# Kernel tuning notes

Measured on AMD Instinct MI355X. Metric: run time of the kernel, lower is better.

## Reference

```python
import jax, jax.numpy as jnp
import numpy as np

B, N_PER, E_PER = 128, 512, 8192          # graphs, nodes/graph, edges/graph
NUM_FEAT, NUM_REL, NUM_BASES = 4, 5, 2
LATENT = [32, 32, 32, 32]
D = 128                                    # sum(LATENT)
MAXN = 50                                  # self.max_neighbor
MAX_WALKS = 21
NUM_CLASSES = 5


def setup_inputs() -> dict:
    key = jax.random.key(0)
    ks = jax.random.split(key, 16)
    N, E = B * N_PER, B * E_PER
    # one-hot node-label features; node 0 of each graph = target user ([1,0,0,0]),
    # node 1 = target item ([0,1,0,0]), rest labels in {2,3}
    labels = jax.random.randint(ks[0], (B, N_PER), 2, NUM_FEAT)
    labels = labels.at[:, 0].set(0).at[:, 1].set(1)
    x = jax.nn.one_hot(labels.reshape(-1), NUM_FEAT, dtype=jnp.float32)
    offs = (jnp.arange(B, dtype=jnp.int32) * N_PER)[:, None]
    src = (jax.random.randint(ks[1], (B, E_PER), 0, N_PER).astype(jnp.int32) + offs).reshape(-1)
    dst = (jax.random.randint(ks[2], (B, E_PER), 0, N_PER).astype(jnp.int32) + offs).reshape(-1)
    edge_index = jnp.stack([src, dst])                       # [2, E] graph-local blocks
    edge_type = jax.random.randint(ks[3], (E,), 0, NUM_REL).astype(jnp.int32)
    batch = jnp.repeat(jnp.arange(B, dtype=jnp.int32), N_PER)
    inp = dict(x=x, edge_index=edge_index, edge_type=edge_type, batch=batch)
    dims = [NUM_FEAT] + LATENT
    ki = 4
    for l in range(4):
        fin, fout = dims[l], dims[l + 1]
        s = 1.0 / np.sqrt(fin)
        inp[f"basis{l}"] = (jax.random.normal(ks[ki], (NUM_BASES, fin, fout)) * s).astype(jnp.float32)
        inp[f"comp{l}"] = (jax.random.normal(ks[ki + 1], (NUM_REL, NUM_BASES)) * 0.5).astype(jnp.float32)
        inp[f"root{l}"] = (jax.random.normal(ks[ki + 2], (fin, fout)) * s).astype(jnp.float32)
        inp[f"cbias{l}"] = jnp.zeros((fout,), jnp.float32)
        ki += 3
    k2 = jax.random.split(jax.random.key(1), 4)
    inp["walk_w"] = (jax.random.normal(k2[0], (MAXN, D)) / np.sqrt(D)).astype(jnp.float32)
    inp["walk_b"] = jnp.zeros((MAXN,), jnp.float32)
    inp["lin1_w"] = (jax.random.normal(k2[1], (128, D)) / np.sqrt(D)).astype(jnp.float32)
    inp["lin1_b"] = jnp.zeros((128,), jnp.float32)
    inp["lin2_w"] = (jax.random.normal(k2[2], (NUM_CLASSES, 128)) / np.sqrt(128.0)).astype(jnp.float32)
    inp["lin2_b"] = jnp.zeros((NUM_CLASSES,), jnp.float32)
    return inp


def _rgcn(h, src, dst, etype, basis, comp, root, bias, n):
    # RGCNConv with basis decomposition: W_r = sum_b comp[r,b] * basis[b]; mean aggregation.
    hs = h[src]                                   # [E, fin]
    ce = comp[etype]                              # [E, num_bases]
    msg = ce[:, 0:1] * (hs @ basis[0])
    for b in range(1, NUM_BASES):
        msg = msg + ce[:, b:b + 1] * (hs @ basis[b])
    agg = jax.ops.segment_sum(msg, dst, num_segments=n)
    deg = jax.ops.segment_sum(jnp.ones(src.shape, msg.dtype), dst, num_segments=n)
    return agg / jnp.maximum(deg, 1.0)[:, None] + h @ root + bias


def _neighbor_table(src, dst, n):
    # per-node sorted out-neighbor lists, padded to MAXN with sentinel n
    E = src.shape[0]
    order = jnp.lexsort((dst, src))               # sort by src, then dst (== torch.sort of neighbors)
    s, d = src[order], dst[order]
    deg = jax.ops.segment_sum(jnp.ones((E,), jnp.int32), src, num_segments=n)
    offs = jnp.cumsum(deg) - deg
    rank = jnp.arange(E, dtype=jnp.int32) - offs[s]
    col = jnp.where(rank < MAXN, rank, MAXN)      # overflow -> dummy column
    table = jnp.full((n, MAXN + 1), n, jnp.int32).at[s, col].set(d)
    return table[:, :MAXN], deg


def _walk(xg, nbr, deg, start, end, w, b):
    # naive_reasoning_walking for one graph: xg [n,D], nbr [n,MAXN] local (pad=n), deg [n]
    n = xg.shape[0]
    trav0 = jnp.zeros((n,), bool).at[start].set(True)

    def step(state, _):
        node, acc, trav, done = state
        nb = jnp.clip(nbr[node], 0, n - 1)        # pads clipped; masked out below
        cnt = deg[node]
        no_nbr = cnt == 0
        logits = w @ acc + b                      # naive_walking_lin1(accumulated)
        valid = (jnp.arange(MAXN) < cnt) & ~trav[nb]
        sel = nb[jnp.argmax(jnp.where(valid, logits, -jnp.inf))]
        acc_new = acc + jnp.where(no_nbr, xg[end], xg[sel])
        upd = ~done
        move = upd & ~no_nbr
        acc = jnp.where(upd, acc_new, acc)
        trav = jnp.where(move, trav.at[sel].set(True), trav)
        done = done | (upd & (no_nbr | (sel == end)))
        node = jnp.where(move, sel, node)
        return (node, acc, trav, done), None

    (_, acc, trav, _), _ = jax.lax.scan(
        step, (start, xg[start], trav0, jnp.array(False)), None, length=MAX_WALKS)
    return acc / trav.sum().astype(acc.dtype)


def _forward(x, edge_index, edge_type, convs, walk_w, walk_b, lin1_w, lin1_b, lin2_w, lin2_b):
    N = x.shape[0]
    src, dst = edge_index[0], edge_index[1]
    h, states = x, []
    for basis, comp, root, bias in convs:
        h = jnp.tanh(_rgcn(h, src, dst, edge_type, basis, comp, root, bias, N))
        states.append(h)
    cs = jnp.concatenate(states, axis=1)          # [N, 128]
    table, deg = _neighbor_table(src, dst, N)
    # graphs are equal-sized (N_PER nodes each) -> per-graph local view
    tab = table.reshape(B, N_PER, MAXN)
    goff = (jnp.arange(B, dtype=jnp.int32) * N_PER)[:, None, None]
    tab_l = jnp.where(tab == N, N_PER, tab - goff)
    deg_l = deg.reshape(B, N_PER)
    xg = cs.reshape(B, N_PER, -1)
    start_l = jnp.argmax(x[:, 0].reshape(B, N_PER), axis=1)   # target user per graph
    end_l = jnp.argmax(x[:, 1].reshape(B, N_PER), axis=1)     # target item per graph
    pooled = jax.vmap(_walk, in_axes=(0, 0, 0, 0, 0, None, None))(
        xg, tab_l, deg_l, start_l, end_l, walk_w, walk_b)      # [B, 128]
    hid = jax.nn.relu(pooled @ lin1_w.T + lin1_b)              # dropout off (eval)
    logits = hid @ lin2_w.T + lin2_b
    return jax.nn.log_softmax(logits, axis=-1)


def reference(x, edge_index, edge_type, batch,
              basis0, comp0, root0, cbias0, basis1, comp1, root1, cbias1,
              basis2, comp2, root2, cbias2, basis3, comp3, root3, cbias3,
              walk_w, walk_b, lin1_w, lin1_b, lin2_w, lin2_b):
    # batch is implied by the fixed graph size; kept for interface fidelity
    convs = [(basis0, comp0, root0, cbias0), (basis1, comp1, root1, cbias1),
             (basis2, comp2, root2, cbias2), (basis3, comp3, root3, cbias3)]
    return _forward(x, edge_index, edge_type, convs,
                    walk_w, walk_b, lin1_w, lin1_b, lin2_w, lin2_b)
```

## Files before the change

kernel.cpp:

```cpp
#include <hip/hip_runtime.h>
#include <math.h>

#define NGRAPH 128
#define NPER   512
#define EPER   8192
#define NFEAT  4
#define NREL   5
#define DD     128
#define MAXNB  50
#define MAXW   21
#define NCLS   5

typedef unsigned short ushortT;
typedef unsigned char ucharT;

#define NTA 1024

__device__ __forceinline__ void scanExcl(const int* cnt, int* offs, int* tA,
                                         int* tB, int tid) {
  if (tid < NPER) tA[tid] = cnt[tid];
  __syncthreads();
  int* a = tA; int* b = tB;
  for (int d = 1; d < NPER; d <<= 1) {
    if (tid < NPER) {
      int v = a[tid];
      if (tid >= d) v += a[tid - d];
      b[tid] = v;
    }
    __syncthreads();
    int* t = a; a = b; b = t;
  }
  if (tid < NPER) offs[tid] = a[tid] - cnt[tid];
  __syncthreads();
}

__global__ __launch_bounds__(NTA, 1)
void build_csr2(const int* __restrict__ esrc, const int* __restrict__ edst,
                const int* __restrict__ etype, const float* __restrict__ x,
                ushortT* __restrict__ gBin, ushortT* __restrict__ gOut,
                int* __restrict__ pIn, int* __restrict__ pOut,
                int* __restrict__ gSE) {
  __shared__ int keyS[EPER];
  __shared__ int auxS[EPER];
  __shared__ ushortT nodS[EPER];
  __shared__ ucharT etyS[EPER];
  __shared__ int cnt[NPER], offs[NPER], fill[NPER];
  __shared__ int se[2];
  const int bid = blockIdx.x, tid = threadIdx.x;
  const int half = bid >> 7;
  const int g = bid & 127;
  const int nbase = g * NPER, ebase = g * EPER;

  if (tid < NPER) { cnt[tid] = 0; fill[tid] = 0; }
  if (tid < 2) se[tid] = NPER;
  __syncthreads();

  if (half == 0) {
    for (int e = tid; e < EPER; e += NTA) {
      auxS[e] = esrc[ebase + e] - nbase;
      etyS[e] = (ucharT)etype[ebase + e];
      int d = edst[ebase + e] - nbase;
      atomicAdd(&cnt[d], 1);
    }
    __syncthreads();
    scanExcl(cnt, offs, keyS, keyS + NPER, tid);
    for (int e = tid; e < EPER; e += NTA) {
      int d = edst[ebase + e] - nbase;
      int pos = offs[d] + atomicAdd(&fill[d], 1);
      keyS[pos] = (d << 13) | e;
    }
    __syncthreads();
    for (int p = tid; p < EPER; p += NTA) {
      const int k = keyS[p];
      const int n = k >> 13;
      const int o = offs[n], c = cnt[n];
      int r = 0;
      for (int i = 0; i < c; ++i) r += (keyS[o + i] < k);
      const int e = k & (EPER - 1);
      gBin[(size_t)g * EPER + o + r] = (ushortT)((auxS[e] << 3) | (int)etyS[e]);
    }
    if (tid < NPER) pIn[nbase + tid] = (offs[tid] << 14) | cnt[tid];
  } else {
    for (int e = tid; e < EPER; e += NTA) {
      int s = esrc[ebase + e] - nbase;
      auxS[e] = s;
      atomicAdd(&cnt[s], 1);
    }
    if (tid < NPER) {
      if (x[(size_t)(nbase + tid) * NFEAT + 0] > 0.5f) atomicMin(&se[0], tid);
      if (x[(size_t)(nbase + tid) * NFEAT + 1] > 0.5f) atomicMin(&se[1], tid);
    }
    __syncthreads();
    scanExcl(cnt, offs, keyS, keyS + NPER, tid);
    for (int e = tid; e < EPER; e += NTA) {
      int s = auxS[e];
      int d = edst[ebase + e] - nbase;
      int pos = offs[s] + atomicAdd(&fill[s], 1);
      keyS[pos] = (d << 13) | e;
      nodS[pos] = (ushortT)s;
    }
    __syncthreads();
    for (int p = tid; p < EPER; p += NTA) {
      const int k = keyS[p];
      const int n = (int)nodS[p];
      const int o = offs[n], c = cnt[n];
      int r = 0;
      for (int i = 0; i < c; ++i) r += (keyS[o + i] < k);
      gOut[(size_t)g * EPER + o + r] = (ushortT)(k >> 13);
    }
    if (tid < NPER) pOut[nbase + tid] = (offs[tid] << 14) | cnt[tid];
    if (tid < 2) gSE[g * 2 + tid] = (se[tid] >= NPER) ? 0 : se[tid];
  }
}

template <int FIN>
__global__ __launch_bounds__(512, 1)
void rgcn_layer2(const float* __restrict__ x, float* __restrict__ cs,
                 const ushortT* __restrict__ gBin, const int* __restrict__ pIn,
                 const float* __restrict__ bas, const float* __restrict__ cmp,
                 const float* __restrict__ rt, const float* __restrict__ bi,
                 int l) {
  constexpr int NK4 = (3 * FIN) / 4;
  constexpr int LPN = FIN / 4;
  __shared__ float A_s[NK4 * 256 * 4];
  __shared__ float Bt_s[NK4 * 32 * 4];
  __shared__ float compS[NREL * 2];
  const int bid = blockIdx.x, tid = threadIdx.x;
  const int g = bid >> 1, half = bid & 1;
  const int nbase = g * NPER;
  const int nb2 = nbase + half * 256;

  for (int idx = tid; idx < NK4 * 128; idx += 512) {
    const int k4 = idx >> 7, rem = idx & 127;
    const int o = rem >> 2, c = rem & 3;
    const int k = k4 * 4 + c;
    float v;
    if (k < FIN) v = bas[k * 32 + o];
    else if (k < 2 * FIN) v = bas[(FIN + (k - FIN)) * 32 + o];
    else v = rt[(k - 2 * FIN) * 32 + o];
    Bt_s[(k4 * 32 + o) * 4 + c] = v;
  }
  if (tid < NREL * 2) compS[tid] = cmp[tid];
  for (int idx = tid; idx < 256 * LPN; idx += 512) {
    const int n = idx / LPN, kq = idx % LPN;
    float4 hv;
    if constexpr (FIN == 4)
      hv = *(const float4*)(x + (size_t)(nb2 + n) * NFEAT);
    else
      hv = *(const float4*)(cs + (size_t)(nb2 + n) * DD + (l - 1) * 32 + kq * 4);
    *(float4*)&A_s[((2 * LPN + kq) * 256 + n) * 4] = hv;
  }
  __syncthreads();

  for (int t = tid; t < 256 * LPN; t += 512) {
    const int n = t / LPN, q = t % LPN;
    const int pk = pIn[nb2 + n];
    const int off = pk >> 14, c = pk & 16383;
    const float inv = 1.0f / (float)(c > 1 ? c : 1);
    float4 s0 = make_float4(0.f, 0.f, 0.f, 0.f);
    float4 s1 = make_float4(0.f, 0.f, 0.f, 0.f);
    const ushortT* el = gBin + (size_t)g * EPER + off;
    for (int i = 0; i < c; ++i) {
      const int pe = (int)el[i];
      const int s = pe >> 3, r = pe & 7;
      float4 hv;
      if constexpr (FIN == 4)
        hv = *(const float4*)(x + (size_t)(nbase + s) * NFEAT);
      else
        hv = *(const float4*)(cs + (size_t)(nbase + s) * DD + (l - 1) * 32 + q * 4);
      const float c0 = compS[r * 2 + 0], c1 = compS[r * 2 + 1];
      s0.x = fmaf(c0, hv.x, s0.x); s0.y = fmaf(c0, hv.y, s0.y);
      s0.z = fmaf(c0, hv.z, s0.z); s0.w = fmaf(c0, hv.w, s0.w);
      s1.x = fmaf(c1, hv.x, s1.x); s1.y = fmaf(c1, hv.y, s1.y);
      s1.z = fmaf(c1, hv.z, s1.z); s1.w = fmaf(c1, hv.w, s1.w);
    }
    s0.x *= inv; s0.y *= inv; s0.z *= inv; s0.w *= inv;
    s1.x *= inv; s1.y *= inv; s1.z *= inv; s1.w *= inv;
    *(float4*)&A_s[(q * 256 + n) * 4] = s0;
    *(float4*)&A_s[((LPN + q) * 256 + n) * 4] = s1;
  }
  __syncthreads();

  const int ot = (tid >> 4) & 3;
  const int nt = (tid & 15) | ((tid >> 6) << 4);
  const int n0 = 2 * nt, o0 = 8 * ot;
  float acc[2][8];
#pragma unroll
  for (int i = 0; i < 2; ++i)
#pragma unroll
    for (int j = 0; j < 8; ++j) acc[i][j] = 0.f;
  for (int k4 = 0; k4 < NK4; ++k4) {
    const float4 a0 = *(const float4*)&A_s[(k4 * 256 + n0) * 4];
    const float4 a1 = *(const float4*)&A_s[(k4 * 256 + n0 + 1) * 4];
#pragma unroll
    for (int j = 0; j < 8; ++j) {
      const float4 b = *(const float4*)&Bt_s[(k4 * 32 + o0 + j) * 4];
      acc[0][j] = fmaf(a0.x, b.x, acc[0][j]);
      acc[0][j] = fmaf(a0.y, b.y, acc[0][j]);
      acc[0][j] = fmaf(a0.z, b.z, acc[0][j]);
      acc[0][j] = fmaf(a0.w, b.w, acc[0][j]);
      acc[1][j] = fmaf(a1.x, b.x, acc[1][j]);
      acc[1][j] = fmaf(a1.y, b.y, acc[1][j]);
      acc[1][j] = fmaf(a1.z, b.z, acc[1][j]);
      acc[1][j] = fmaf(a1.w, b.w, acc[1][j]);
    }
  }
#pragma unroll
  for (int i = 0; i < 2; ++i) {
    float4 w0, w1;
    w0.x = tanhf(acc[i][0] + bi[o0 + 0]); w0.y = tanhf(acc[i][1] + bi[o0 + 1]);
    w0.z = tanhf(acc[i][2] + bi[o0 + 2]); w0.w = tanhf(acc[i][3] + bi[o0 + 3]);
    w1.x = tanhf(acc[i][4] + bi[o0 + 4]); w1.y = tanhf(acc[i][5] + bi[o0 + 5]);
    w1.z = tanhf(acc[i][6] + bi[o0 + 6]); w1.w = tanhf(acc[i][7] + bi[o0 + 7]);
    float* dst = cs + (size_t)(nb2 + n0 + i) * DD + l * 32 + o0;
    *(float4*)dst = w0;
    *(float4*)(dst + 4) = w1;
  }
}

__global__ __launch_bounds__(256, 1)
void walk_head(const float* __restrict__ cs, const ushortT* __restrict__ gOut,
               const int* __restrict__ pOut, const int* __restrict__ gSE,
               const float* __restrict__ walk_w, const float* __restrict__ walk_b,
               const float* __restrict__ lin1_w, const float* __restrict__ lin1_b,
               const float* __restrict__ lin2_w, const float* __restrict__ lin2_b,
               float* __restrict__ out) {
  __shared__ float wT[DD * 65];
  __shared__ float wb[64];
  __shared__ float accS[DD];
  __shared__ float part[4 * 64];
  __shared__ int trav[NPER];
  __shared__ float pooledS[DD], hidS[DD], logitsS[8];
  __shared__ int scal[8];
  const int g = blockIdx.x, tid = threadIdx.x;
  const int nbase = g * NPER;

  for (int i = tid; i < DD * 64; i += 256) {
    const int j = i >> 7, k = i & 127;
    wT[k * 65 + j] = walk_w[j * DD + k];
  }
  if (tid < 64) {
    wb[tid] = (tid < MAXNB) ? walk_b[tid] : 0.f;
    for (int k = 0; k < DD; ++k)
      if (tid >= MAXNB) wT[k * 65 + tid] = 0.f;
  }
  for (int i = tid; i < NPER; i += 256) trav[i] = 0;
  __syncthreads();
  const int startN = gSE[2 * g];
  const int endN = gSE[2 * g + 1];
  if (tid == 0) { scal[0] = startN; scal[1] = 0; scal[6] = 0; trav[startN] = 1; }
  if (tid < DD) accS[tid] = cs[(size_t)(nbase + startN) * DD + tid];
  __syncthreads();

  for (int step = 0; step < MAXW; ++step) {
    {
      const int w = tid >> 6, j = tid & 63, k0 = w * 32;
      float s = 0.f;
#pragma unroll
      for (int k = 0; k < 32; ++k) s += wT[(k0 + k) * 65 + j] * accS[k0 + k];
      part[w * 64 + j] = s;
    }
    __syncthreads();
    if (tid < 64) {
      const int j = tid;
      float lg = part[j] + part[64 + j] + part[128 + j] + part[192 + j];
      lg += wb[j];
      const int node = scal[0];
      const int pk = pOut[nbase + node];
      const int off = pk >> 14, c = pk & 16383;
      const int jmax = (c < MAXNB) ? c : MAXNB;
      float myval = -INFINITY;
      if (j < jmax) {
        const int nb = (int)gOut[(size_t)g * EPER + off + j];
        if (!trav[nb]) myval = lg;
      }
      int myidx = j;
#pragma unroll
      for (int o = 1; o < 64; o <<= 1) {
        const float ov = __shfl_xor(myval, o, 64);
        const int oi = __shfl_xor(myidx, o, 64);
        if (ov > myval || (ov == myval && oi < myidx)) { myval = ov; myidx = oi; }
      }
      if (j == 0) {
        const int done = scal[1];
        const int no_nbr = (c == 0);
        int sel = no_nbr ? (NPER - 1) : (int)gOut[(size_t)g * EPER + off + myidx];
        const int upd = !done;
        const int move = upd && !no_nbr;
        scal[2] = upd;
        scal[3] = no_nbr ? endN : sel;
        if (move) trav[sel] = 1;
        if (upd && (no_nbr || sel == endN)) scal[1] = 1;
        if (move) scal[0] = sel;
      }
    }
    __syncthreads();
    if (scal[2] && tid < DD) accS[tid] += cs[(size_t)(nbase + scal[3]) * DD + tid];
    __syncthreads();
  }

  for (int i = tid; i < NPER; i += 256)
    if (trav[i]) atomicAdd(&scal[6], 1);
  __syncthreads();
  {
    const float tc = (float)scal[6];
    if (tid < DD) pooledS[tid] = accS[tid] / tc;
  }
  __syncthreads();
  if (tid < DD) {
    const float4* w4 = (const float4*)(lin1_w + (size_t)tid * DD);
    float s = lin1_b[tid];
#pragma unroll 8
    for (int k4 = 0; k4 < DD / 4; ++k4) {
      const float4 wv = w4[k4];
      s += wv.x * pooledS[k4 * 4 + 0] + wv.y * pooledS[k4 * 4 + 1]
         + wv.z * pooledS[k4 * 4 + 2] + wv.w * pooledS[k4 * 4 + 3];
    }
    hidS[tid] = fmaxf(s, 0.f);
  }
  __syncthreads();
  if (tid < NCLS) {
    const float4* w4 = (const float4*)(lin2_w + (size_t)tid * DD);
    float s = lin2_b[tid];
#pragma unroll 8
    for (int k4 = 0; k4 < DD / 4; ++k4) {
      const float4 wv = w4[k4];
      s += wv.x * hidS[k4 * 4 + 0] + wv.y * hidS[k4 * 4 + 1]
         + wv.z * hidS[k4 * 4 + 2] + wv.w * hidS[k4 * 4 + 3];
    }
    logitsS[tid] = s;
  }
  __syncthreads();
  if (tid < NCLS) {
    float m = logitsS[0];
    for (int c = 1; c < NCLS; ++c) m = fmaxf(m, logitsS[c]);
    float sum = 0.f;
    for (int c = 0; c < NCLS; ++c) sum += expf(logitsS[c] - m);
    const float lse = m + logf(sum);
    out[g * NCLS + tid] = logitsS[tid] - lse;
  }
}

extern "C" void kernel_launch(void* const* d_in, const int* in_sizes, int n_in,
                              void* d_out, int out_size, void* d_ws, size_t ws_size,
                              hipStream_t stream) {
  const float* x = (const float*)d_in[0];
  const int* ei = (const int*)d_in[1];
  const int E = in_sizes[1] / 2;
  const int* esrc = ei;
  const int* edst = ei + E;
  const int* et = (const int*)d_in[2];

  char* ws = (char*)d_ws;
  float* cs = (float*)ws;
  size_t off = (size_t)NGRAPH * NPER * DD * sizeof(float);
  ushortT* gBin = (ushortT*)(ws + off); off += (size_t)NGRAPH * EPER * sizeof(ushortT);
  ushortT* gOut = (ushortT*)(ws + off); off += (size_t)NGRAPH * EPER * sizeof(ushortT);
  int* pIn = (int*)(ws + off); off += (size_t)NGRAPH * NPER * sizeof(int);
  int* pOut = (int*)(ws + off); off += (size_t)NGRAPH * NPER * sizeof(int);
  int* gSE = (int*)(ws + off); off += (size_t)NGRAPH * 2 * sizeof(int);

  build_csr2<<<dim3(2 * NGRAPH), dim3(NTA), 0, stream>>>(esrc, edst, et, x, gBin,
                                                         gOut, pIn, pOut, gSE);
  rgcn_layer2<NFEAT><<<dim3(2 * NGRAPH), dim3(512), 0, stream>>>(
      x, cs, gBin, pIn, (const float*)d_in[4], (const float*)d_in[5],
      (const float*)d_in[6], (const float*)d_in[7], 0);
  rgcn_layer2<32><<<dim3(2 * NGRAPH), dim3(512), 0, stream>>>(
      x, cs, gBin, pIn, (const float*)d_in[8], (const float*)d_in[9],
      (const float*)d_in[10], (const float*)d_in[11], 1);
  rgcn_layer2<32><<<dim3(2 * NGRAPH), dim3(512), 0, stream>>>(
      x, cs, gBin, pIn, (const float*)d_in[12], (const float*)d_in[13],
      (const float*)d_in[14], (const float*)d_in[15], 2);
  rgcn_layer2<32><<<dim3(2 * NGRAPH), dim3(512), 0, stream>>>(
      x, cs, gBin, pIn, (const float*)d_in[16], (const float*)d_in[17],
      (const float*)d_in[18], (const float*)d_in[19], 3);
  walk_head<<<dim3(NGRAPH), dim3(256), 0, stream>>>(
      cs, gOut, pOut, gSE, (const float*)d_in[20], (const float*)d_in[21],
      (const float*)d_in[22], (const float*)d_in[23], (const float*)d_in[24],
      (const float*)d_in[25], (float*)d_out);
}
```

Measured before the change: 178.6 us.

## Split RGCN layers into smaller blocks, unroll gathers, prefetch walk candidates

The RGCN layer kernel now processes 64 nodes per 256-thread block (8 blocks per graph) instead of 256 nodes per 512-thread block, giving more blocks and better occupancy. The neighbor gather loop is unrolled by four so several loads are in flight at once. The walk kernel stages its graph's CSR arrays in shared memory and prefetches all candidate neighbor feature rows into a scratch buffer while the logits matvec runs, which takes the dependent global read off the serial per-step critical path. It also skips that work once the walk is done. The cost is much more shared memory per walk block and redundant prefetch traffic for neighbors that are not chosen.

```diff
diff --git a/kernel.cpp b/kernel.cpp
--- a/kernel.cpp
+++ b/kernel.cpp
@@ -113,46 +113,46 @@
   }
 }
 
+#define NPB 64
 template <int FIN>
-__global__ __launch_bounds__(512, 1)
-void rgcn_layer2(const float* __restrict__ x, float* __restrict__ cs,
+__global__ __launch_bounds__(256)
+void rgcn_layer3(const float* __restrict__ x, float* __restrict__ cs,
                  const ushortT* __restrict__ gBin, const int* __restrict__ pIn,
                  const float* __restrict__ bas, const float* __restrict__ cmp,
                  const float* __restrict__ rt, const float* __restrict__ bi,
                  int l) {
   constexpr int NK4 = (3 * FIN) / 4;
   constexpr int LPN = FIN / 4;
-  __shared__ float A_s[NK4 * 256 * 4];
+  __shared__ float A_s[NK4 * NPB * 4];
   __shared__ float Bt_s[NK4 * 32 * 4];
   __shared__ float compS[NREL * 2];
   const int bid = blockIdx.x, tid = threadIdx.x;
-  const int g = bid >> 1, half = bid & 1;
+  const int g = bid >> 3, blk = bid & 7;
   const int nbase = g * NPER;
-  const int nb2 = nbase + half * 256;
-
-  for (int idx = tid; idx < NK4 * 128; idx += 512) {
+  const int nb2 = nbase + blk * NPB;
+
+  for (int idx = tid; idx < NK4 * 128; idx += 256) {
     const int k4 = idx >> 7, rem = idx & 127;
     const int o = rem >> 2, c = rem & 3;
     const int k = k4 * 4 + c;
     float v;
-    if (k < FIN) v = bas[k * 32 + o];
-    else if (k < 2 * FIN) v = bas[(FIN + (k - FIN)) * 32 + o];
+    if (k < 2 * FIN) v = bas[k * 32 + o];
     else v = rt[(k - 2 * FIN) * 32 + o];
     Bt_s[(k4 * 32 + o) * 4 + c] = v;
   }
   if (tid < NREL * 2) compS[tid] = cmp[tid];
-  for (int idx = tid; idx < 256 * LPN; idx += 512) {
+  for (int idx = tid; idx < NPB * LPN; idx += 256) {
     const int n = idx / LPN, kq = idx % LPN;
     float4 hv;
     if constexpr (FIN == 4)
       hv = *(const float4*)(x + (size_t)(nb2 + n) * NFEAT);
     else
       hv = *(const float4*)(cs + (size_t)(nb2 + n) * DD + (l - 1) * 32 + kq * 4);
-    *(float4*)&A_s[((2 * LPN + kq) * 256 + n) * 4] = hv;
-  }
-  __syncthreads();
-
-  for (int t = tid; t < 256 * LPN; t += 512) {
+    *(float4*)&A_s[((2 * LPN + kq) * NPB + n) * 4] = hv;
+  }
+  __syncthreads();
+
+  for (int t = tid; t < NPB * LPN; t += 256) {
     const int n = t / LPN, q = t % LPN;
     const int pk = pIn[nb2 + n];
     const int off = pk >> 14, c = pk & 16383;
@@ -160,15 +160,44 @@
     float4 s0 = make_float4(0.f, 0.f, 0.f, 0.f);
     float4 s1 = make_float4(0.f, 0.f, 0.f, 0.f);
     const ushortT* el = gBin + (size_t)g * EPER + off;
-    for (int i = 0; i < c; ++i) {
+    const float* hb;
+    int stride;
+    if constexpr (FIN == 4) { hb = x + (size_t)nbase * NFEAT; stride = NFEAT; }
+    else { hb = cs + (size_t)nbase * DD + (l - 1) * 32 + q * 4; stride = DD; }
+    int i = 0;
+    for (; i + 4 <= c; i += 4) {
+      const int p0 = (int)el[i + 0], p1 = (int)el[i + 1];
+      const int p2 = (int)el[i + 2], p3 = (int)el[i + 3];
+      const float4 h0 = *(const float4*)(hb + (size_t)(p0 >> 3) * stride);
+      const float4 h1 = *(const float4*)(hb + (size_t)(p1 >> 3) * stride);
+      const float4 h2 = *(const float4*)(hb + (size_t)(p2 >> 3) * stride);
+      const float4 h3 = *(const float4*)(hb + (size_t)(p3 >> 3) * stride);
+      float c0, c1;
+      c0 = compS[(p0 & 7) * 2]; c1 = compS[(p0 & 7) * 2 + 1];
+      s0.x = fmaf(c0, h0.x, s0.x); s0.y = fmaf(c0, h0.y, s0.y);
+      s0.z = fmaf(c0, h0.z, s0.z); s0.w = fmaf(c0, h0.w, s0.w);
+      s1.x = fmaf(c1, h0.x, s1.x); s1.y = fmaf(c1, h0.y, s1.y);
+      s1.z = fmaf(c1, h0.z, s1.z); s1.w = fmaf(c1, h0.w, s1.w);
+      c0 = compS[(p1 & 7) * 2]; c1 = compS[(p1 & 7) * 2 + 1];
+      s0.x = fmaf(c0, h1.x, s0.x); s0.y = fmaf(c0, h1.y, s0.y);
+      s0.z = fmaf(c0, h1.z, s0.z); s0.w = fmaf(c0, h1.w, s0.w);
+      s1.x = fmaf(c1, h1.x, s1.x); s1.y = fmaf(c1, h1.y, s1.y);
+      s1.z = fmaf(c1, h1.z, s1.z); s1.w = fmaf(c1, h1.w, s1.w);
+      c0 = compS[(p2 & 7) * 2]; c1 = compS[(p2 & 7) * 2 + 1];
+      s0.x = fmaf(c0, h2.x, s0.x); s0.y = fmaf(c0, h2.y, s0.y);
+      s0.z = fmaf(c0, h2.z, s0.z); s0.w = fmaf(c0, h2.w, s0.w);
+      s1.x = fmaf(c1, h2.x, s1.x); s1.y = fmaf(c1, h2.y, s1.y);
+      s1.z = fmaf(c1, h2.z, s1.z); s1.w = fmaf(c1, h2.w, s1.w);
+      c0 = compS[(p3 & 7) * 2]; c1 = compS[(p3 & 7) * 2 + 1];
+      s0.x = fmaf(c0, h3.x, s0.x); s0.y = fmaf(c0, h3.y, s0.y);
+      s0.z = fmaf(c0, h3.z, s0.z); s0.w = fmaf(c0, h3.w, s0.w);
+      s1.x = fmaf(c1, h3.x, s1.x); s1.y = fmaf(c1, h3.y, s1.y);
+      s1.z = fmaf(c1, h3.z, s1.z); s1.w = fmaf(c1, h3.w, s1.w);
+    }
+    for (; i < c; ++i) {
       const int pe = (int)el[i];
-      const int s = pe >> 3, r = pe & 7;
-      float4 hv;
-      if constexpr (FIN == 4)
-        hv = *(const float4*)(x + (size_t)(nbase + s) * NFEAT);
-      else
-        hv = *(const float4*)(cs + (size_t)(nbase + s) * DD + (l - 1) * 32 + q * 4);
-      const float c0 = compS[r * 2 + 0], c1 = compS[r * 2 + 1];
+      const float4 hv = *(const float4*)(hb + (size_t)(pe >> 3) * stride);
+      const float c0 = compS[(pe & 7) * 2], c1 = compS[(pe & 7) * 2 + 1];
       s0.x = fmaf(c0, hv.x, s0.x); s0.y = fmaf(c0, hv.y, s0.y);
       s0.z = fmaf(c0, hv.z, s0.z); s0.w = fmaf(c0, hv.w, s0.w);
       s1.x = fmaf(c1, hv.x, s1.x); s1.y = fmaf(c1, hv.y, s1.y);
@@ -176,24 +205,24 @@
     }
     s0.x *= inv; s0.y *= inv; s0.z *= inv; s0.w *= inv;
     s1.x *= inv; s1.y *= inv; s1.z *= inv; s1.w *= inv;
-    *(float4*)&A_s[(q * 256 + n) * 4] = s0;
-    *(float4*)&A_s[((LPN + q) * 256 + n) * 4] = s1;
-  }
-  __syncthreads();
-
-  const int ot = (tid >> 4) & 3;
-  const int nt = (tid & 15) | ((tid >> 6) << 4);
-  const int n0 = 2 * nt, o0 = 8 * ot;
-  float acc[2][8];
+    *(float4*)&A_s[(q * NPB + n) * 4] = s0;
+    *(float4*)&A_s[((LPN + q) * NPB + n) * 4] = s1;
+  }
+  __syncthreads();
+
+  const int ot = (tid >> 5) & 7;
+  const int nt = tid & 31;
+  const int n0 = 2 * nt, o0 = 4 * ot;
+  float acc[2][4];
 #pragma unroll
   for (int i = 0; i < 2; ++i)
 #pragma unroll
-    for (int j = 0; j < 8; ++j) acc[i][j] = 0.f;
+    for (int j = 0; j < 4; ++j) acc[i][j] = 0.f;
   for (int k4 = 0; k4 < NK4; ++k4) {
-    const float4 a0 = *(const float4*)&A_s[(k4 * 256 + n0) * 4];
-    const float4 a1 = *(const float4*)&A_s[(k4 * 256 + n0 + 1) * 4];
-#pragma unroll
-    for (int j = 0; j < 8; ++j) {
+    const float4 a0 = *(const float4*)&A_s[(k4 * NPB + n0) * 4];
+    const float4 a1 = *(const float4*)&A_s[(k4 * NPB + n0 + 1) * 4];
+#pragma unroll
+    for (int j = 0; j < 4; ++j) {
       const float4 b = *(const float4*)&Bt_s[(k4 * 32 + o0 + j) * 4];
       acc[0][j] = fmaf(a0.x, b.x, acc[0][j]);
       acc[0][j] = fmaf(a0.y, b.y, acc[0][j]);
@@ -207,33 +236,35 @@
   }
 #pragma unroll
   for (int i = 0; i < 2; ++i) {
-    float4 w0, w1;
-    w0.x = tanhf(acc[i][0] + bi[o0 + 0]); w0.y = tanhf(acc[i][1] + bi[o0 + 1]);
-    w0.z = tanhf(acc[i][2] + bi[o0 + 2]); w0.w = tanhf(acc[i][3] + bi[o0 + 3]);
-    w1.x = tanhf(acc[i][4] + bi[o0 + 4]); w1.y = tanhf(acc[i][5] + bi[o0 + 5]);
-    w1.z = tanhf(acc[i][6] + bi[o0 + 6]); w1.w = tanhf(acc[i][7] + bi[o0 + 7]);
-    float* dst = cs + (size_t)(nb2 + n0 + i) * DD + l * 32 + o0;
-    *(float4*)dst = w0;
-    *(float4*)(dst + 4) = w1;
+    float4 w0;
+    w0.x = tanhf(acc[i][0] + bi[o0 + 0]);
+    w0.y = tanhf(acc[i][1] + bi[o0 + 1]);
+    w0.z = tanhf(acc[i][2] + bi[o0 + 2]);
+    w0.w = tanhf(acc[i][3] + bi[o0 + 3]);
+    *(float4*)(cs + (size_t)(nb2 + n0 + i) * DD + l * 32 + o0) = w0;
   }
 }
 
 __global__ __launch_bounds__(256, 1)
-void walk_head(const float* __restrict__ cs, const ushortT* __restrict__ gOut,
-               const int* __restrict__ pOut, const int* __restrict__ gSE,
-               const float* __restrict__ walk_w, const float* __restrict__ walk_b,
-               const float* __restrict__ lin1_w, const float* __restrict__ lin1_b,
-               const float* __restrict__ lin2_w, const float* __restrict__ lin2_b,
-               float* __restrict__ out) {
+void walk_head2(const float* __restrict__ cs, const ushortT* __restrict__ gOut,
+                const int* __restrict__ pOut, const int* __restrict__ gSE,
+                const float* __restrict__ walk_w, const float* __restrict__ walk_b,
+                const float* __restrict__ lin1_w, const float* __restrict__ lin1_b,
+                const float* __restrict__ lin2_w, const float* __restrict__ lin2_b,
+                float* __restrict__ out) {
   __shared__ float wT[DD * 65];
   __shared__ float wb[64];
+  __shared__ ushortT gOutS[EPER];
+  __shared__ int pOutS[NPER];
+  __shared__ int trav[NPER];
+  __shared__ float scratch[MAXNB * DD];
   __shared__ float accS[DD];
   __shared__ float part[4 * 64];
-  __shared__ int trav[NPER];
-  __shared__ float pooledS[DD], hidS[DD], logitsS[8];
+  __shared__ float hidS[DD], pooledS[DD], logitsS[8];
   __shared__ int scal[8];
   const int g = blockIdx.x, tid = threadIdx.x;
   const int nbase = g * NPER;
+  const float4* cs4 = (const float4*)cs;
 
   for (int i = tid; i < DD * 64; i += 256) {
     const int j = i >> 7, k = i & 127;
@@ -244,7 +275,15 @@
     for (int k = 0; k < DD; ++k)
       if (tid >= MAXNB) wT[k * 65 + tid] = 0.f;
   }
-  for (int i = tid; i < NPER; i += 256) trav[i] = 0;
+  {
+    const unsigned int* g32 = (const unsigned int*)(gOut + (size_t)g * EPER);
+    unsigned int* s32 = (unsigned int*)gOutS;
+    for (int i = tid; i < EPER / 2; i += 256) s32[i] = g32[i];
+    for (int i = tid; i < NPER; i += 256) {
+      pOutS[i] = pOut[nbase + i];
+      trav[i] = 0;
+    }
+  }
   __syncthreads();
   const int startN = gSE[2 * g];
   const int endN = gSE[2 * g + 1];
@@ -253,25 +292,54 @@
   __syncthreads();
 
   for (int step = 0; step < MAXW; ++step) {
-    {
-      const int w = tid >> 6, j = tid & 63, k0 = w * 32;
-      float s = 0.f;
-#pragma unroll
-      for (int k = 0; k < 32; ++k) s += wT[(k0 + k) * 65 + j] * accS[k0 + k];
-      part[w * 64 + j] = s;
-    }
-    __syncthreads();
-    if (tid < 64) {
+    const int doneF = scal[1];
+    int jmax = 0;
+    if (!doneF) {
+      const int node = scal[0];
+      const int pk = pOutS[node];
+      const int off = pk >> 14, c = pk & 16383;
+      jmax = (c < MAXNB) ? c : MAXNB;
+      const int nq = jmax * 32;
+      float4 pf0, pf1, pf2, pf3, pf4, pf5, pf6;
+      const int q0 = tid, q1 = tid + 256, q2 = tid + 512, q3 = tid + 768;
+      const int q4 = tid + 1024, q5 = tid + 1280, q6 = tid + 1536;
+      if (q0 < nq) pf0 = cs4[(size_t)(nbase + (int)gOutS[off + (q0 >> 5)]) * 32 + (q0 & 31)];
+      if (q1 < nq) pf1 = cs4[(size_t)(nbase + (int)gOutS[off + (q1 >> 5)]) * 32 + (q1 & 31)];
+      if (q2 < nq) pf2 = cs4[(size_t)(nbase + (int)gOutS[off + (q2 >> 5)]) * 32 + (q2 & 31)];
+      if (q3 < nq) pf3 = cs4[(size_t)(nbase + (int)gOutS[off + (q3 >> 5)]) * 32 + (q3 & 31)];
+      if (q4 < nq) pf4 = cs4[(size_t)(nbase + (int)gOutS[off + (q4 >> 5)]) * 32 + (q4 & 31)];
+      if (q5 < nq) pf5 = cs4[(size_t)(nbase + (int)gOutS[off + (q5 >> 5)]) * 32 + (q5 & 31)];
+      if (q6 < nq) pf6 = cs4[(size_t)(nbase + (int)gOutS[off + (q6 >> 5)]) * 32 + (q6 & 31)];
+      {
+        const int w = tid >> 6, j = tid & 63, k0 = w * 32;
+        float s = 0.f;
+#pragma unroll
+        for (int k = 0; k < 32; ++k) s += wT[(k0 + k) * 65 + j] * accS[k0 + k];
+        part[w * 64 + j] = s;
+      }
+      float4* scr4 = (float4*)scratch;
+      if (q0 < nq) scr4[q0] = pf0;
+      if (q1 < nq) scr4[q1] = pf1;
+      if (q2 < nq) scr4[q2] = pf2;
+      if (q3 < nq) scr4[q3] = pf3;
+      if (q4 < nq) scr4[q4] = pf4;
+      if (q5 < nq) scr4[q5] = pf5;
+      if (q6 < nq) scr4[q6] = pf6;
+    }
+    __syncthreads();
+    if (doneF) {
+      if (tid == 0) scal[2] = 0;
+    } else if (tid < 64) {
       const int j = tid;
       float lg = part[j] + part[64 + j] + part[128 + j] + part[192 + j];
       lg += wb[j];
       const int node = scal[0];
-      const int pk = pOut[nbase + node];
+      const int pk = pOutS[node];
       const int off = pk >> 14, c = pk & 16383;
-      const int jmax = (c < MAXNB) ? c : MAXNB;
+      const int jm = (c < MAXNB) ? c : MAXNB;
       float myval = -INFINITY;
-      if (j < jmax) {
-        const int nb = (int)gOut[(size_t)g * EPER + off + j];
+      if (j < jm) {
+        const int nb = (int)gOutS[off + j];
         if (!trav[nb]) myval = lg;
       }
       int myidx = j;
@@ -282,20 +350,21 @@
         if (ov > myval || (ov == myval && oi < myidx)) { myval = ov; myidx = oi; }
       }
       if (j == 0) {
-        const int done = scal[1];
         const int no_nbr = (c == 0);
-        int sel = no_nbr ? (NPER - 1) : (int)gOut[(size_t)g * EPER + off + myidx];
-        const int upd = !done;
-        const int move = upd && !no_nbr;
-        scal[2] = upd;
+        const int sel = no_nbr ? (NPER - 1) : (int)gOutS[off + myidx];
+        scal[2] = 1;
         scal[3] = no_nbr ? endN : sel;
-        if (move) trav[sel] = 1;
-        if (upd && (no_nbr || sel == endN)) scal[1] = 1;
-        if (move) scal[0] = sel;
+        scal[4] = no_nbr ? -1 : myidx;
+        if (!no_nbr) { trav[sel] = 1; scal[0] = sel; }
+        if (no_nbr || sel == endN) scal[1] = 1;
       }
     }
     __syncthreads();
-    if (scal[2] && tid < DD) accS[tid] += cs[(size_t)(nbase + scal[3]) * DD + tid];
+    if (scal[2] && tid < DD) {
+      const int si = scal[4];
+      if (si >= 0) accS[tid] += scratch[si * DD + tid];
+      else accS[tid] += cs[(size_t)(nbase + scal[3]) * DD + tid];
+    }
     __syncthreads();
   }
 
@@ -362,19 +431,19 @@
 
   build_csr2<<<dim3(2 * NGRAPH), dim3(NTA), 0, stream>>>(esrc, edst, et, x, gBin,
                                                          gOut, pIn, pOut, gSE);
-  rgcn_layer2<NFEAT><<<dim3(2 * NGRAPH), dim3(512), 0, stream>>>(
+  rgcn_layer3<NFEAT><<<dim3(8 * NGRAPH), dim3(256), 0, stream>>>(
       x, cs, gBin, pIn, (const float*)d_in[4], (const float*)d_in[5],
       (const float*)d_in[6], (const float*)d_in[7], 0);
-  rgcn_layer2<32><<<dim3(2 * NGRAPH), dim3(512), 0, stream>>>(
+  rgcn_layer3<32><<<dim3(8 * NGRAPH), dim3(256), 0, stream>>>(
       x, cs, gBin, pIn, (const float*)d_in[8], (const float*)d_in[9],
       (const float*)d_in[10], (const float*)d_in[11], 1);
-  rgcn_layer2<32><<<dim3(2 * NGRAPH), dim3(512), 0, stream>>>(
+  rgcn_layer3<32><<<dim3(8 * NGRAPH), dim3(256), 0, stream>>>(
       x, cs, gBin, pIn, (const float*)d_in[12], (const float*)d_in[13],
       (const float*)d_in[14], (const float*)d_in[15], 2);
-  rgcn_layer2<32><<<dim3(2 * NGRAPH), dim3(512), 0, stream>>>(
+  rgcn_layer3<32><<<dim3(8 * NGRAPH), dim3(256), 0, stream>>>(
       x, cs, gBin, pIn, (const float*)d_in[16], (const float*)d_in[17],
       (const float*)d_in[18], (const float*)d_in[19], 3);
-  walk_head<<<dim3(NGRAPH), dim3(256), 0, stream>>>(
+  walk_head2<<<dim3(NGRAPH), dim3(256), 0, stream>>>(
       cs, gOut, pOut, gSE, (const float*)d_in[20], (const float*)d_in[21],
       (const float*)d_in[22], (const float*)d_in[23], (const float*)d_in[24],
       (const float*)d_in[25], (float*)d_out);
```

Measured after the change: 525.1 us. +194.0%, slower.

## Prefetch candidate neighbor features and stage adjacency in LDS for walk

Applied to the files above, without the earlier changes.

The walk kernel now copies the graph's outgoing adjacency and offsets into shared memory. At each step it speculatively loads the feature rows of all up-to-50 candidate neighbors into a shared scratch buffer while the logit matvec runs, so the selected row can be accumulated from LDS instead of a dependent global load. It also skips the matvec once the walk is done. This targets the serialized global-load latency chain per step, at the cost of much more shared memory (about 25KB scratch plus 16KB adjacency) and extra global traffic for candidates that are not chosen.

```diff
diff --git a/kernel.cpp b/kernel.cpp
--- a/kernel.cpp
+++ b/kernel.cpp
@@ -219,21 +219,25 @@
 }
 
 __global__ __launch_bounds__(256, 1)
-void walk_head(const float* __restrict__ cs, const ushortT* __restrict__ gOut,
-               const int* __restrict__ pOut, const int* __restrict__ gSE,
-               const float* __restrict__ walk_w, const float* __restrict__ walk_b,
-               const float* __restrict__ lin1_w, const float* __restrict__ lin1_b,
-               const float* __restrict__ lin2_w, const float* __restrict__ lin2_b,
-               float* __restrict__ out) {
+void walk_head2(const float* __restrict__ cs, const ushortT* __restrict__ gOut,
+                const int* __restrict__ pOut, const int* __restrict__ gSE,
+                const float* __restrict__ walk_w, const float* __restrict__ walk_b,
+                const float* __restrict__ lin1_w, const float* __restrict__ lin1_b,
+                const float* __restrict__ lin2_w, const float* __restrict__ lin2_b,
+                float* __restrict__ out) {
   __shared__ float wT[DD * 65];
   __shared__ float wb[64];
+  __shared__ ushortT gOutS[EPER];
+  __shared__ int pOutS[NPER];
+  __shared__ int trav[NPER];
+  __shared__ float scratch[MAXNB * DD];
   __shared__ float accS[DD];
   __shared__ float part[4 * 64];
-  __shared__ int trav[NPER];
-  __shared__ float pooledS[DD], hidS[DD], logitsS[8];
+  __shared__ float hidS[DD], pooledS[DD], logitsS[8];
   __shared__ int scal[8];
   const int g = blockIdx.x, tid = threadIdx.x;
   const int nbase = g * NPER;
+  const float4* cs4 = (const float4*)cs;
 
   for (int i = tid; i < DD * 64; i += 256) {
     const int j = i >> 7, k = i & 127;
@@ -244,7 +248,15 @@
     for (int k = 0; k < DD; ++k)
       if (tid >= MAXNB) wT[k * 65 + tid] = 0.f;
   }
-  for (int i = tid; i < NPER; i += 256) trav[i] = 0;
+  {
+    const unsigned int* g32 = (const unsigned int*)(gOut + (size_t)g * EPER);
+    unsigned int* s32 = (unsigned int*)gOutS;
+    for (int i = tid; i < EPER / 2; i += 256) s32[i] = g32[i];
+    for (int i = tid; i < NPER; i += 256) {
+      pOutS[i] = pOut[nbase + i];
+      trav[i] = 0;
+    }
+  }
   __syncthreads();
   const int startN = gSE[2 * g];
   const int endN = gSE[2 * g + 1];
@@ -253,25 +265,54 @@
   __syncthreads();
 
   for (int step = 0; step < MAXW; ++step) {
-    {
-      const int w = tid >> 6, j = tid & 63, k0 = w * 32;
-      float s = 0.f;
-#pragma unroll
-      for (int k = 0; k < 32; ++k) s += wT[(k0 + k) * 65 + j] * accS[k0 + k];
-      part[w * 64 + j] = s;
-    }
-    __syncthreads();
-    if (tid < 64) {
+    const int doneF = scal[1];
+    int jmax = 0;
+    if (!doneF) {
+      const int node = scal[0];
+      const int pk = pOutS[node];
+      const int off = pk >> 14, c = pk & 16383;
+      jmax = (c < MAXNB) ? c : MAXNB;
+      const int nq = jmax * 32;
+      float4 pf0, pf1, pf2, pf3, pf4, pf5, pf6;
+      const int q0 = tid, q1 = tid + 256, q2 = tid + 512, q3 = tid + 768;
+      const int q4 = tid + 1024, q5 = tid + 1280, q6 = tid + 1536;
+      if (q0 < nq) pf0 = cs4[(size_t)(nbase + (int)gOutS[off + (q0 >> 5)]) * 32 + (q0 & 31)];
+      if (q1 < nq) pf1 = cs4[(size_t)(nbase + (int)gOutS[off + (q1 >> 5)]) * 32 + (q1 & 31)];
+      if (q2 < nq) pf2 = cs4[(size_t)(nbase + (int)gOutS[off + (q2 >> 5)]) * 32 + (q2 & 31)];
+      if (q3 < nq) pf3 = cs4[(size_t)(nbase + (int)gOutS[off + (q3 >> 5)]) * 32 + (q3 & 31)];
+      if (q4 < nq) pf4 = cs4[(size_t)(nbase + (int)gOutS[off + (q4 >> 5)]) * 32 + (q4 & 31)];
+      if (q5 < nq) pf5 = cs4[(size_t)(nbase + (int)gOutS[off + (q5 >> 5)]) * 32 + (q5 & 31)];
+      if (q6 < nq) pf6 = cs4[(size_t)(nbase + (int)gOutS[off + (q6 >> 5)]) * 32 + (q6 & 31)];
+      {
+        const int w = tid >> 6, j = tid & 63, k0 = w * 32;
+        float s = 0.f;
+#pragma unroll
+        for (int k = 0; k < 32; ++k) s += wT[(k0 + k) * 65 + j] * accS[k0 + k];
+        part[w * 64 + j] = s;
+      }
+      float4* scr4 = (float4*)scratch;
+      if (q0 < nq) scr4[q0] = pf0;
+      if (q1 < nq) scr4[q1] = pf1;
+      if (q2 < nq) scr4[q2] = pf2;
+      if (q3 < nq) scr4[q3] = pf3;
+      if (q4 < nq) scr4[q4] = pf4;
+      if (q5 < nq) scr4[q5] = pf5;
+      if (q6 < nq) scr4[q6] = pf6;
+    }
+    __syncthreads();
+    if (doneF) {
+      if (tid == 0) scal[2] = 0;
+    } else if (tid < 64) {
       const int j = tid;
       float lg = part[j] + part[64 + j] + part[128 + j] + part[192 + j];
       lg += wb[j];
       const int node = scal[0];
-      const int pk = pOut[nbase + node];
+      const int pk = pOutS[node];
       const int off = pk >> 14, c = pk & 16383;
-      const int jmax = (c < MAXNB) ? c : MAXNB;
+      const int jm = (c < MAXNB) ? c : MAXNB;
       float myval = -INFINITY;
-      if (j < jmax) {
-        const int nb = (int)gOut[(size_t)g * EPER + off + j];
+      if (j < jm) {
+        const int nb = (int)gOutS[off + j];
         if (!trav[nb]) myval = lg;
       }
       int myidx = j;
@@ -282,20 +323,21 @@
         if (ov > myval || (ov == myval && oi < myidx)) { myval = ov; myidx = oi; }
       }
       if (j == 0) {
-        const int done = scal[1];
         const int no_nbr = (c == 0);
-        int sel = no_nbr ? (NPER - 1) : (int)gOut[(size_t)g * EPER + off + myidx];
-        const int upd = !done;
-        const int move = upd && !no_nbr;
-        scal[2] = upd;
+        const int sel = no_nbr ? (NPER - 1) : (int)gOutS[off + myidx];
+        scal[2] = 1;
         scal[3] = no_nbr ? endN : sel;
-        if (move) trav[sel] = 1;
-        if (upd && (no_nbr || sel == endN)) scal[1] = 1;
-        if (move) scal[0] = sel;
+        scal[4] = no_nbr ? -1 : myidx;
+        if (!no_nbr) { trav[sel] = 1; scal[0] = sel; }
+        if (no_nbr || sel == endN) scal[1] = 1;
       }
     }
     __syncthreads();
-    if (scal[2] && tid < DD) accS[tid] += cs[(size_t)(nbase + scal[3]) * DD + tid];
+    if (scal[2] && tid < DD) {
+      const int si = scal[4];
+      if (si >= 0) accS[tid] += scratch[si * DD + tid];
+      else accS[tid] += cs[(size_t)(nbase + scal[3]) * DD + tid];
+    }
     __syncthreads();
   }
 
@@ -374,7 +416,7 @@
   rgcn_layer2<32><<<dim3(2 * NGRAPH), dim3(512), 0, stream>>>(
       x, cs, gBin, pIn, (const float*)d_in[16], (const float*)d_in[17],
       (const float*)d_in[18], (const float*)d_in[19], 3);
-  walk_head<<<dim3(NGRAPH), dim3(256), 0, stream>>>(
+  walk_head2<<<dim3(NGRAPH), dim3(256), 0, stream>>>(
       cs, gOut, pOut, gSE, (const float*)d_in[20], (const float*)d_in[21],
       (const float*)d_in[22], (const float*)d_in[23], (const float*)d_in[24],
       (const float*)d_in[25], (float*)d_out);
```

Result: no change. 178.2 us (-0.2%).

## Precompute per-node walk logits and run walk in one wavefront; prefetch gathers

Applied to the files above, without the earlier changes.

The walk head now multiplies every node's 128-d feature by the walk weight once up front. Because the running sum of features is linear, each step's logits become a running sum of these per-node rows. The serial 21-step walk then runs inside a single 64-lane wavefront with adjacency and offsets staged in shared memory, removing the per-step block barriers and matvecs, and pooling is done afterwards from the recorded node list. The RGCN aggregation loop also software-prefetches the next neighbor's features, and the basis load is simplified. In exchange every node's logits are computed even though only the visited ones are needed, and the change relies on linearity and may alter float summation order.

```diff
diff --git a/kernel.cpp b/kernel.cpp
--- a/kernel.cpp
+++ b/kernel.cpp
@@ -115,11 +115,11 @@
 
 template <int FIN>
 __global__ __launch_bounds__(512, 1)
-void rgcn_layer2(const float* __restrict__ x, float* __restrict__ cs,
-                 const ushortT* __restrict__ gBin, const int* __restrict__ pIn,
-                 const float* __restrict__ bas, const float* __restrict__ cmp,
-                 const float* __restrict__ rt, const float* __restrict__ bi,
-                 int l) {
+void rgcn_layer2p(const float* __restrict__ x, float* __restrict__ cs,
+                  const ushortT* __restrict__ gBin, const int* __restrict__ pIn,
+                  const float* __restrict__ bas, const float* __restrict__ cmp,
+                  const float* __restrict__ rt, const float* __restrict__ bi,
+                  int l) {
   constexpr int NK4 = (3 * FIN) / 4;
   constexpr int LPN = FIN / 4;
   __shared__ float A_s[NK4 * 256 * 4];
@@ -135,8 +135,7 @@
     const int o = rem >> 2, c = rem & 3;
     const int k = k4 * 4 + c;
     float v;
-    if (k < FIN) v = bas[k * 32 + o];
-    else if (k < 2 * FIN) v = bas[(FIN + (k - FIN)) * 32 + o];
+    if (k < 2 * FIN) v = bas[k * 32 + o];
     else v = rt[(k - 2 * FIN) * 32 + o];
     Bt_s[(k4 * 32 + o) * 4 + c] = v;
   }
@@ -160,15 +159,24 @@
     float4 s0 = make_float4(0.f, 0.f, 0.f, 0.f);
     float4 s1 = make_float4(0.f, 0.f, 0.f, 0.f);
     const ushortT* el = gBin + (size_t)g * EPER + off;
-    for (int i = 0; i < c; ++i) {
-      const int pe = (int)el[i];
-      const int s = pe >> 3, r = pe & 7;
-      float4 hv;
-      if constexpr (FIN == 4)
-        hv = *(const float4*)(x + (size_t)(nbase + s) * NFEAT);
-      else
-        hv = *(const float4*)(cs + (size_t)(nbase + s) * DD + (l - 1) * 32 + q * 4);
-      const float c0 = compS[r * 2 + 0], c1 = compS[r * 2 + 1];
+    const float* hb;
+    if constexpr (FIN == 4) hb = x + (size_t)nbase * NFEAT;
+    else hb = cs + (size_t)nbase * DD + (l - 1) * 32 + q * 4;
+    constexpr int STRIDE = (FIN == 4) ? NFEAT : DD;
+    if (c > 0) {
+      int pe = (int)el[0];
+      float4 hv = *(const float4*)(hb + (size_t)(pe >> 3) * STRIDE);
+      for (int i = 0; i + 1 < c; ++i) {
+        const int pe_n = (int)el[i + 1];
+        const float4 hv_n = *(const float4*)(hb + (size_t)(pe_n >> 3) * STRIDE);
+        const float c0 = compS[(pe & 7) * 2], c1 = compS[(pe & 7) * 2 + 1];
+        s0.x = fmaf(c0, hv.x, s0.x); s0.y = fmaf(c0, hv.y, s0.y);
+        s0.z = fmaf(c0, hv.z, s0.z); s0.w = fmaf(c0, hv.w, s0.w);
+        s1.x = fmaf(c1, hv.x, s1.x); s1.y = fmaf(c1, hv.y, s1.y);
+        s1.z = fmaf(c1, hv.z, s1.z); s1.w = fmaf(c1, hv.w, s1.w);
+        pe = pe_n; hv = hv_n;
+      }
+      const float c0 = compS[(pe & 7) * 2], c1 = compS[(pe & 7) * 2 + 1];
       s0.x = fmaf(c0, hv.x, s0.x); s0.y = fmaf(c0, hv.y, s0.y);
       s0.z = fmaf(c0, hv.z, s0.z); s0.w = fmaf(c0, hv.w, s0.w);
       s1.x = fmaf(c1, hv.x, s1.x); s1.y = fmaf(c1, hv.y, s1.y);
@@ -218,61 +226,83 @@
   }
 }
 
-__global__ __launch_bounds__(256, 1)
-void walk_head(const float* __restrict__ cs, const ushortT* __restrict__ gOut,
-               const int* __restrict__ pOut, const int* __restrict__ gSE,
-               const float* __restrict__ walk_w, const float* __restrict__ walk_b,
-               const float* __restrict__ lin1_w, const float* __restrict__ lin1_b,
-               const float* __restrict__ lin2_w, const float* __restrict__ lin2_b,
-               float* __restrict__ out) {
-  __shared__ float wT[DD * 65];
-  __shared__ float wb[64];
-  __shared__ float accS[DD];
-  __shared__ float part[4 * 64];
-  __shared__ int trav[NPER];
+__global__ __launch_bounds__(512, 1)
+void walk_head3(const float* __restrict__ cs, const ushortT* __restrict__ gOut,
+                const int* __restrict__ pOut, const int* __restrict__ gSE,
+                const float* __restrict__ walk_w, const float* __restrict__ walk_b,
+                const float* __restrict__ lin1_w, const float* __restrict__ lin1_b,
+                const float* __restrict__ lin2_w, const float* __restrict__ lin2_b,
+                float* __restrict__ out) {
+  __shared__ float PS[NPER * 52];
+  __shared__ float wS[52 * 128];
+  __shared__ int travS[NPER];
+  __shared__ int listS[MAXW + 2];
+  __shared__ int scal[8];
   __shared__ float pooledS[DD], hidS[DD], logitsS[8];
-  __shared__ int scal[8];
   const int g = blockIdx.x, tid = threadIdx.x;
   const int nbase = g * NPER;
 
-  for (int i = tid; i < DD * 64; i += 256) {
+  for (int i = tid; i < 52 * 128; i += 512) {
     const int j = i >> 7, k = i & 127;
-    wT[k * 65 + j] = walk_w[j * DD + k];
-  }
-  if (tid < 64) {
-    wb[tid] = (tid < MAXNB) ? walk_b[tid] : 0.f;
-    for (int k = 0; k < DD; ++k)
-      if (tid >= MAXNB) wT[k * 65 + tid] = 0.f;
-  }
-  for (int i = tid; i < NPER; i += 256) trav[i] = 0;
-  __syncthreads();
+    wS[i] = (j < MAXNB) ? walk_w[j * DD + k] : 0.f;
+  }
+  __syncthreads();
+
+  {
+    const int n = tid;
+    const float4* xrow = (const float4*)(cs + (size_t)(nbase + n) * DD);
+    float4 accq[13];
+#pragma unroll
+    for (int jq = 0; jq < 13; ++jq) accq[jq] = make_float4(0.f, 0.f, 0.f, 0.f);
+    for (int k4 = 0; k4 < 32; ++k4) {
+      const float4 a = xrow[k4];
+#pragma unroll
+      for (int jq = 0; jq < 13; ++jq) {
+        const float4 w0 = *(const float4*)&wS[(jq * 4 + 0) * 128 + k4 * 4];
+        const float4 w1 = *(const float4*)&wS[(jq * 4 + 1) * 128 + k4 * 4];
+        const float4 w2 = *(const float4*)&wS[(jq * 4 + 2) * 128 + k4 * 4];
+        const float4 w3 = *(const float4*)&wS[(jq * 4 + 3) * 128 + k4 * 4];
+        accq[jq].x = fmaf(a.w, w0.w, fmaf(a.z, w0.z, fmaf(a.y, w0.y, fmaf(a.x, w0.x, accq[jq].x))));
+        accq[jq].y = fmaf(a.w, w1.w, fmaf(a.z, w1.z, fmaf(a.y, w1.y, fmaf(a.x, w1.x, accq[jq].y))));
+        accq[jq].z = fmaf(a.w, w2.w, fmaf(a.z, w2.z, fmaf(a.y, w2.y, fmaf(a.x, w2.x, accq[jq].z))));
+        accq[jq].w = fmaf(a.w, w3.w, fmaf(a.z, w3.z, fmaf(a.y, w3.y, fmaf(a.x, w3.x, accq[jq].w))));
+      }
+    }
+#pragma unroll
+    for (int jq = 0; jq < 13; ++jq)
+      *(float4*)&PS[n * 52 + jq * 4] = accq[jq];
+  }
+  __syncthreads();
+
+  ushortT* gOutS = (ushortT*)wS;
+  int* pOutS = (int*)(wS + 4096);
+  {
+    const unsigned int* g32 = (const unsigned int*)(gOut + (size_t)g * EPER);
+    unsigned int* s32 = (unsigned int*)gOutS;
+    for (int i = tid; i < EPER / 2; i += 512) s32[i] = g32[i];
+    for (int i = tid; i < NPER; i += 512) {
+      pOutS[i] = pOut[nbase + i];
+      travS[i] = 0;
+    }
+  }
   const int startN = gSE[2 * g];
   const int endN = gSE[2 * g + 1];
-  if (tid == 0) { scal[0] = startN; scal[1] = 0; scal[6] = 0; trav[startN] = 1; }
-  if (tid < DD) accS[tid] = cs[(size_t)(nbase + startN) * DD + tid];
-  __syncthreads();
-
-  for (int step = 0; step < MAXW; ++step) {
-    {
-      const int w = tid >> 6, j = tid & 63, k0 = w * 32;
-      float s = 0.f;
-#pragma unroll
-      for (int k = 0; k < 32; ++k) s += wT[(k0 + k) * 65 + j] * accS[k0 + k];
-      part[w * 64 + j] = s;
-    }
-    __syncthreads();
-    if (tid < 64) {
-      const int j = tid;
-      float lg = part[j] + part[64 + j] + part[128 + j] + part[192 + j];
-      lg += wb[j];
-      const int node = scal[0];
-      const int pk = pOut[nbase + node];
+  if (tid == 0) { travS[startN] = 1; listS[0] = startN; }
+  __syncthreads();
+
+  if (tid < 64) {
+    const int j = tid;
+    float l = 0.f;
+    if (j < MAXNB) l = PS[startN * 52 + j] + walk_b[j];
+    int node = startN, visited = 1, nrows = 1;
+    for (int step = 0; step < MAXW; ++step) {
+      const int pk = pOutS[node];
       const int off = pk >> 14, c = pk & 16383;
-      const int jmax = (c < MAXNB) ? c : MAXNB;
+      const int jm = (c < MAXNB) ? c : MAXNB;
       float myval = -INFINITY;
-      if (j < jmax) {
-        const int nb = (int)gOut[(size_t)g * EPER + off + j];
-        if (!trav[nb]) myval = lg;
+      if (j < jm) {
+        const int nb = (int)gOutS[off + j];
+        if (!travS[nb]) myval = l;
       }
       int myidx = j;
 #pragma unroll
@@ -281,30 +311,29 @@
         const int oi = __shfl_xor(myidx, o, 64);
         if (ov > myval || (ov == myval && oi < myidx)) { myval = ov; myidx = oi; }
       }
-      if (j == 0) {
-        const int done = scal[1];
-        const int no_nbr = (c == 0);
-        int sel = no_nbr ? (NPER - 1) : (int)gOut[(size_t)g * EPER + off + myidx];
-        const int upd = !done;
-        const int move = upd && !no_nbr;
-        scal[2] = upd;
-        scal[3] = no_nbr ? endN : sel;
-        if (move) trav[sel] = 1;
-        if (upd && (no_nbr || sel == endN)) scal[1] = 1;
-        if (move) scal[0] = sel;
+      const bool no_nbr = (c == 0);
+      const int sel = no_nbr ? 0 : (int)gOutS[off + myidx];
+      const int tgt = no_nbr ? endN : sel;
+      if (j == 0) listS[nrows] = tgt;
+      nrows++;
+      if (j < MAXNB) l += PS[tgt * 52 + j];
+      if (!no_nbr) {
+        if (j == 0) travS[sel] = 1;
+        visited++;
+        node = sel;
       }
-    }
-    __syncthreads();
-    if (scal[2] && tid < DD) accS[tid] += cs[(size_t)(nbase + scal[3]) * DD + tid];
-    __syncthreads();
-  }
-
-  for (int i = tid; i < NPER; i += 256)
-    if (trav[i]) atomicAdd(&scal[6], 1);
-  __syncthreads();
-  {
-    const float tc = (float)scal[6];
-    if (tid < DD) pooledS[tid] = accS[tid] / tc;
+      if (no_nbr || sel == endN) break;
+    }
+    if (j == 0) { scal[0] = nrows; scal[1] = visited; }
+  }
+  __syncthreads();
+
+  const int nrows = scal[0];
+  if (tid < DD) {
+    float acc = cs[(size_t)(nbase + listS[0]) * DD + tid];
+    for (int t = 1; t < nrows; ++t)
+      acc += cs[(size_t)(nbase + listS[t]) * DD + tid];
+    pooledS[tid] = acc / (float)scal[1];
   }
   __syncthreads();
   if (tid < DD) {
@@ -362,19 +391,19 @@
 
   build_csr2<<<dim3(2 * NGRAPH), dim3(NTA), 0, stream>>>(esrc, edst, et, x, gBin,
                                                          gOut, pIn, pOut, gSE);
-  rgcn_layer2<NFEAT><<<dim3(2 * NGRAPH), dim3(512), 0, stream>>>(
+  rgcn_layer2p<NFEAT><<<dim3(2 * NGRAPH), dim3(512), 0, stream>>>(
       x, cs, gBin, pIn, (const float*)d_in[4], (const float*)d_in[5],
       (const float*)d_in[6], (const float*)d_in[7], 0);
-  rgcn_layer2<32><<<dim3(2 * NGRAPH), dim3(512), 0, stream>>>(
+  rgcn_layer2p<32><<<dim3(2 * NGRAPH), dim3(512), 0, stream>>>(
       x, cs, gBin, pIn, (const float*)d_in[8], (const float*)d_in[9],
       (const float*)d_in[10], (const float*)d_in[11], 1);
-  rgcn_layer2<32><<<dim3(2 * NGRAPH), dim3(512), 0, stream>>>(
+  rgcn_layer2p<32><<<dim3(2 * NGRAPH), dim3(512), 0, stream>>>(
       x, cs, gBin, pIn, (const float*)d_in[12], (const float*)d_in[13],
       (const float*)d_in[14], (const float*)d_in[15], 2);
-  rgcn_layer2<32><<<dim3(2 * NGRAPH), dim3(512), 0, stream>>>(
+  rgcn_layer2p<32><<<dim3(2 * NGRAPH), dim3(512), 0, stream>>>(
       x, cs, gBin, pIn, (const float*)d_in[16], (const float*)d_in[17],
       (const float*)d_in[18], (const float*)d_in[19], 3);
-  walk_head<<<dim3(NGRAPH), dim3(256), 0, stream>>>(
+  walk_head3<<<dim3(NGRAPH), dim3(512), 0, stream>>>(
       cs, gOut, pOut, gSE, (const float*)d_in[20], (const float*)d_in[21],
       (const float*)d_in[22], (const float*)d_in[23], (const float*)d_in[24],
       (const float*)d_in[25], (float*)d_out);
```

Measured after the change: 201.0 us. +12.5%, slower.
